# Kernel tuning notes

Measured on AMD Instinct MI355X. Metric: run time of the kernel, lower is better.

The kernel has to match this reference:

```python
import jax, jax.numpy as jnp
import numpy as np

EMBED_DIM = 2048
NUM_HEADS = 16
HEAD_DIM = EMBED_DIM // NUM_HEADS
BATCH = 4
SEQ = 1024
ROPE_BASE = 10000.0


def _rotate_half(x):
    x1, x2 = jnp.split(x, 2, axis=-1)
    return jnp.concatenate([-x2, x1], axis=-1)


def setup_inputs() -> dict:
    key = jax.random.key(0)
    ks = jax.random.split(key, 8)
    query = jax.random.normal(ks[0], (BATCH, SEQ, EMBED_DIM), dtype=jnp.float32)
    kkey = jax.random.normal(ks[1], (BATCH, SEQ, EMBED_DIM), dtype=jnp.float32)
    value = jax.random.normal(ks[2], (BATCH, SEQ, EMBED_DIM), dtype=jnp.float32)
    # causal mask: scores.masked_fill(mask == 0, -inf)
    mask = jnp.tril(jnp.ones((SEQ, SEQ), dtype=jnp.int32))[None, None]
    # RoPE tables [S, head_dim]
    inv_freq = 1.0 / (ROPE_BASE ** (np.arange(0, HEAD_DIM, 2, dtype=np.float32) / HEAD_DIM))
    pos = np.arange(SEQ, dtype=np.float32)
    freqs = np.outer(pos, inv_freq)                      # [S, D/2]
    emb = np.concatenate([freqs, freqs], axis=-1)        # [S, D]
    rope_cos = jnp.asarray(np.cos(emb), dtype=jnp.float32)
    rope_sin = jnp.asarray(np.sin(emb), dtype=jnp.float32)
    s = 1.0 / np.sqrt(EMBED_DIM)
    Wq = jax.random.normal(ks[3], (EMBED_DIM, EMBED_DIM), dtype=jnp.float32) * s
    Wk = jax.random.normal(ks[4], (EMBED_DIM, EMBED_DIM), dtype=jnp.float32) * s
    Wv = jax.random.normal(ks[5], (EMBED_DIM, EMBED_DIM), dtype=jnp.float32) * s
    Wo = jax.random.normal(ks[6], (EMBED_DIM, EMBED_DIM), dtype=jnp.float32) * s
    return {"query": query, "key": kkey, "value": value, "mask": mask,
            "rope_cos": rope_cos, "rope_sin": rope_sin,
            "Wq": Wq, "Wk": Wk, "Wv": Wv, "Wo": Wo}


def reference(query, key, value, mask, rope_cos, rope_sin, Wq, Wk, Wv, Wo):
    B, S, E = query.shape
    # projections (nn.Linear: x @ W.T)
    def proj(x, W):
        y = x @ W.T
        return y.reshape(B, -1, NUM_HEADS, HEAD_DIM).transpose(0, 2, 1, 3)  # [B,H,S,D]
    Q = proj(query, Wq)
    K = proj(key, Wk)
    V = proj(value, Wv)
    # RoPE (rotate-half form), cos/sin broadcast over batch and heads
    cos = rope_cos[None, None]  # [1,1,S,D]
    sin = rope_sin[None, None]
    Q = Q * cos + _rotate_half(Q) * sin
    K = K * cos + _rotate_half(K) * sin
    scale = jnp.asarray(np.sqrt(HEAD_DIM), dtype=Q.dtype)
    scores = jnp.einsum('bhqd,bhkd->bhqk', Q, K) / scale
    scores = jnp.where(mask == 0, jnp.asarray(-jnp.inf, scores.dtype), scores)
    attn = jax.nn.softmax(scores, axis=-1)
    context = jnp.einsum('bhqk,bhkd->bhqd', attn, V)
    context = context.transpose(0, 2, 1, 3).reshape(B, S, E)
    out = context @ Wo.T
    return out
```

## Files before the change

kernel.cpp:

```cpp
#include <hip/hip_runtime.h>
#include <stdint.h>

#define E_DIM 2048
#define N_HEADS 16
#define H_DIM 128
#define BATCH 4
#define SEQL 1024
#define M_ROWS 4096

typedef __attribute__((ext_vector_type(8))) short bf16x8;
typedef __attribute__((ext_vector_type(4))) float f32x4;

#define AS1 __attribute__((address_space(1)))
#define AS3 __attribute__((address_space(3)))

__device__ __forceinline__ void gload16(const void* g, void* l) {
  __builtin_amdgcn_global_load_lds((const AS1 uint32_t*)g, (AS3 uint32_t*)l, 16, 0, 0);
}

__device__ __forceinline__ unsigned short f2bf(float f) {
  union { float f; uint32_t u; } v; v.f = f;
  return (unsigned short)((v.u + 0x7FFFu + ((v.u >> 16) & 1u)) >> 16);
}

__global__ __launch_bounds__(256) void k_cvt(
    const float* __restrict__ q, const float* __restrict__ k, const float* __restrict__ v,
    const float* __restrict__ wq, const float* __restrict__ wk,
    const float* __restrict__ wv, const float* __restrict__ wo,
    ushort* __restrict__ oq, ushort* __restrict__ ok, ushort* __restrict__ ov,
    ushort* __restrict__ owq, ushort* __restrict__ owk,
    ushort* __restrict__ owv, ushort* __restrict__ owo) {
  int y = blockIdx.y;
  const float* in;
  ushort* out;
  if (y < 3) {
    in = (y == 0) ? q : (y == 1) ? k : v;
    out = (y == 0) ? oq : (y == 1) ? ok : ov;
  } else {
    if (blockIdx.x >= 4096) return;
    in = (y == 3) ? wq : (y == 4) ? wk : (y == 5) ? wv : wo;
    out = (y == 3) ? owq : (y == 4) ? owk : (y == 5) ? owv : owo;
  }
  int i = (blockIdx.x * 256 + threadIdx.x) * 4;
  float4 vv = *reinterpret_cast<const float4*>(in + i);
  *reinterpret_cast<ushort4*>(out + i) =
      make_ushort4(f2bf(vv.x), f2bf(vv.y), f2bf(vv.z), f2bf(vv.w));
}

template <int NREP>
__device__ __forceinline__ void gemm256_mainloop(const ushort* __restrict__ A,
                                                 const ushort* __restrict__ W,
                                                 ushort* lds, int m0, int n0,
                                                 const int browRows[NREP],
                                                 f32x4 (&acc)[8][NREP]) {
  const int tid = threadIdx.x;
  const int w = tid >> 6, lane = tid & 63, quad = lane >> 4, lid = lane & 15;
  constexpr int KTILES = E_DIM / 64;
  constexpr int BELE = NREP * 4096;
  ushort* const bufA = lds;
  ushort* const bufB = lds + 3 * 16384;

  const int r0 = tid >> 3, c0 = (tid & 7) ^ (r0 & 7);
  const int ldw = w * 512;
  const ushort* aB = A + ((size_t)m0 + r0) * E_DIM + c0 * 8;
  const ushort* bB = W + ((size_t)n0 + r0) * E_DIM + c0 * 8;

#define STG(baseP, buf, kt, half)                                              \
  do {                                                                         \
    const ushort* _g = (baseP) + (size_t)(half) * 128 * E_DIM + (kt) * 64;     \
    gload16(_g, (buf) + (half) * 8192 + ldw);                                  \
    gload16(_g + (size_t)64 * E_DIM, (buf) + (half) * 8192 + 4096 + ldw);      \
  } while (0)

  int ofsA[2], ofsB[NREP][2];
  {
    const int rowA = (w >> 2) * 128 + lid;
#pragma unroll
    for (int ks = 0; ks < 2; ++ks)
      ofsA[ks] = rowA * 64 + (((ks * 4 + quad) ^ (lid & 7)) * 8);
#pragma unroll
    for (int ni = 0; ni < NREP; ++ni)
#pragma unroll
      for (int ks = 0; ks < 2; ++ks)
        ofsB[ni][ks] = browRows[ni] * 64 + (((ks * 4 + quad) ^ (lid & 7)) * 8);
  }

  bf16x8 bfr[NREP][2];

#define VMW_STEADY                                                             \
  do {                                                                         \
    if constexpr (NREP == 4)                                                   \
      asm volatile("s_waitcnt vmcnt(8)" ::: "memory");                         \
    else                                                                       \
      asm volatile("s_waitcnt vmcnt(6)" ::: "memory");                         \
  } while (0)

#define PH(aoff, boff, q, STGS, VMW)                                           \
  do {                                                                         \
    bf16x8 af[2][2];                                                           \
    if ((q) == 0) {                                                            \
      _Pragma("unroll") for (int ni = 0; ni < NREP; ++ni)                      \
          _Pragma("unroll") for (int ks = 0; ks < 2; ++ks)                     \
              bfr[ni][ks] = *reinterpret_cast<const bf16x8*>(                  \
                  bufB + (boff) + ofsB[ni][ks]);                               \
    }                                                                          \
    _Pragma("unroll") for (int d = 0; d < 2; ++d)                              \
        _Pragma("unroll") for (int ks = 0; ks < 2; ++ks)                       \
            af[d][ks] = *reinterpret_cast<const bf16x8*>(                      \
                bufA + (aoff) + ofsA[ks] + ((q) * 2 + d) * 1024);              \
    STGS;                                                                      \
    VMW;                                                                       \
    __builtin_amdgcn_s_barrier();                                              \
    asm volatile("s_waitcnt lgkmcnt(0)" ::: "memory");                         \
    __builtin_amdgcn_s_setprio(1);                                             \
    _Pragma("unroll") for (int ks = 0; ks < 2; ++ks)                           \
        _Pragma("unroll") for (int d = 0; d < 2; ++d)                          \
            _Pragma("unroll") for (int ni = 0; ni < NREP; ++ni)                \
                acc[(q) * 2 + d][ni] = __builtin_amdgcn_mfma_f32_16x16x32_bf16(\
                    af[d][ks], bfr[ni][ks], acc[(q) * 2 + d][ni], 0, 0, 0);    \
    __builtin_amdgcn_s_setprio(0);                                             \
    __builtin_amdgcn_s_barrier();                                              \
  } while (0)

  STG(aB, bufA, 0, 0); STG(aB, bufA, 0, 1);
  STG(bB, bufB, 0, 0); if (NREP == 4) STG(bB, bufB, 0, 1);
  STG(aB, bufA + 16384, 1, 0); STG(aB, bufA + 16384, 1, 1);
  STG(bB, bufB + BELE, 1, 0); if (NREP == 4) STG(bB, bufB + BELE, 1, 1);
  VMW_STEADY;
  __builtin_amdgcn_s_barrier();

  int cur = 0, nx2 = 2;
  for (int t = 0; t < KTILES; ++t) {
    const int aoff = cur * 16384;
    const int boff = (t & 1) * BELE;
    ushort* sA = bufA + nx2 * 16384;
    ushort* sB = bufB + boff;
    const bool st = (t < KTILES - 2);
    PH(aoff, boff, 0, if (st) STG(aB, sA, t + 2, 0), );
    PH(aoff, boff, 1, if (st) STG(aB, sA, t + 2, 1), );
    PH(aoff, boff, 2, if (st) STG(bB, sB, t + 2, 0), );
    PH(aoff, boff, 3, if (st && NREP == 4) STG(bB, sB, t + 2, 1),
       if (st) VMW_STEADY;
       else if (t == KTILES - 2)
           asm volatile("s_waitcnt vmcnt(0)" ::: "memory"));
    cur = (cur == 2) ? 0 : cur + 1;
    nx2 = (nx2 == 2) ? 0 : nx2 + 1;
  }
#undef PH
#undef VMW_STEADY
#undef STG
}

__global__ __launch_bounds__(512, 2) void k_gemm_qkv(
    const ushort* __restrict__ xq, const ushort* __restrict__ xk, const ushort* __restrict__ xv,
    const ushort* __restrict__ wq, const ushort* __restrict__ wk, const ushort* __restrict__ wv,
    ushort* __restrict__ Qr, ushort* __restrict__ Kr, ushort* __restrict__ Vr,
    const float* __restrict__ cosT, const float* __restrict__ sinT) {
  extern __shared__ ushort lds[];
  unsigned lin = blockIdx.x + 8u * (blockIdx.y + 16u * blockIdx.z);
  unsigned swz = (lin & 7u) * 48u + (lin >> 3);
  const int bx = swz & 7u;
  const int by = (swz >> 3) & 15u;
  const int z = swz >> 7;

  const ushort* A = (z == 0) ? xq : (z == 1) ? xk : xv;
  const ushort* W = (z == 0) ? wq : (z == 1) ? wk : wv;
  ushort* Out = (z == 0) ? Qr : (z == 1) ? Kr : Vr;
  const int tid = threadIdx.x;
  const int w = tid >> 6, lane = tid & 63, quad = lane >> 4, lid = lane & 15;
  const int wn = w & 3;
  const int n0 = bx * 256;
  const int m0 = by * 256;

  int browRows[4];
#pragma unroll
  for (int ni = 0; ni < 4; ++ni)
    browRows[ni] = (wn >> 1) * 128 + (wn & 1) * 32 + (ni & 1) * 16 + (ni >> 1) * 64 + lid;

  f32x4 acc[8][4];
  const f32x4 z4 = {0.f, 0.f, 0.f, 0.f};
#pragma unroll
  for (int i = 0; i < 8; ++i)
#pragma unroll
    for (int j = 0; j < 4; ++j) acc[i][j] = z4;

  gemm256_mainloop<4>(A, W, lds, m0, n0, browRows, acc);

  const int b = m0 >> 10;
  const int h = bx * 2 + (wn >> 1);
  ushort* Og = Out + (size_t)(b * N_HEADS + h) * SEQL * H_DIM;
  const bool rope = (z < 2);
#pragma unroll
  for (int mi = 0; mi < 8; ++mi)
#pragma unroll
    for (int r = 0; r < 4; ++r) {
      int s = (m0 & (SEQL - 1)) + (w >> 2) * 128 + mi * 16 + quad * 4 + r;
      size_t row = (size_t)s * H_DIM;
      if (rope) {
#pragma unroll
        for (int ni = 0; ni < 2; ++ni) {
          int d0 = (wn & 1) * 32 + ni * 16 + lid;
          float c = cosT[s * H_DIM + d0];
          float sn = sinT[s * H_DIM + d0];
          float x0 = acc[mi][ni][r], x1 = acc[mi][ni + 2][r];
          Og[row + d0]      = f2bf(x0 * c - x1 * sn);
          Og[row + d0 + 64] = f2bf(x1 * c + x0 * sn);
        }
      } else {
#pragma unroll
        for (int ni = 0; ni < 4; ++ni) {
          int d = (wn & 1) * 32 + (ni & 1) * 16 + (ni >> 1) * 64 + lid;
          Og[row + d] = f2bf(acc[mi][ni][r]);
        }
      }
    }
}

__global__ __launch_bounds__(512, 2) void k_gemm_o(const ushort* __restrict__ A,
                                                   const ushort* __restrict__ W,
                                                   float* __restrict__ Out) {
  extern __shared__ ushort lds[];
  unsigned lin = blockIdx.x + 16u * blockIdx.y;
  unsigned swz = (lin & 7u) * 32u + (lin >> 3);
  const int bx = swz & 15u;
  const int by = swz >> 4;

  const int tid = threadIdx.x;
  const int w = tid >> 6, lane = tid & 63, quad = lane >> 4, lid = lane & 15;
  const int wn = w & 3;
  const int n0 = bx * 128;
  const int m0 = by * 256;

  int browRows[2];
#pragma unroll
  for (int ni = 0; ni < 2; ++ni) browRows[ni] = wn * 32 + ni * 16 + lid;

  f32x4 acc[8][2];
  const f32x4 z4 = {0.f, 0.f, 0.f, 0.f};
#pragma unroll
  for (int i = 0; i < 8; ++i)
#pragma unroll
    for (int j = 0; j < 2; ++j) acc[i][j] = z4;

  gemm256_mainloop<2>(A, W, lds, m0, n0, browRows, acc);

#pragma unroll
  for (int mi = 0; mi < 8; ++mi)
#pragma unroll
    for (int r = 0; r < 4; ++r) {
      size_t row = (size_t)(m0 + (w >> 2) * 128 + mi * 16 + quad * 4 + r) * E_DIM + n0;
#pragma unroll
      for (int ni = 0; ni < 2; ++ni) Out[row + browRows[ni]] = acc[mi][ni][r];
    }
}

__global__ __launch_bounds__(256) void k_transv(const ushort* __restrict__ V,
                                                ushort* __restrict__ Vt) {
  __shared__ ushort t[32][33];
  int bh = blockIdx.z;
  int s0 = blockIdx.x * 32;
  int d0 = blockIdx.y * 32;
  int j = threadIdx.x & 31;
  int i = threadIdx.x >> 5;
  for (int rr = 0; rr < 4; ++rr) {
    int row = i + rr * 8;
    t[row][j] = V[((size_t)bh * SEQL + s0 + row) * H_DIM + d0 + j];
  }
  __syncthreads();
  for (int rr = 0; rr < 4; ++rr) {
    int drow = i + rr * 8;
    Vt[((size_t)bh * H_DIM + d0 + drow) * SEQL + s0 + j] = t[j][drow];
  }
}

__global__ __launch_bounds__(256, 2) void k_attn(const ushort* __restrict__ Q,
                                                 const ushort* __restrict__ K,
                                                 const ushort* __restrict__ Vt,
                                                 ushort* __restrict__ Ctx) {
  __shared__ ushort Ks[128 * 128];
  __shared__ ushort Vs[128 * 64];
  __shared__ ushort Ps[4][32 * 40];
  const int tid = threadIdx.x;
  const int w = tid >> 6, lane = tid & 63, quad = lane >> 4, lid = lane & 15;
  const int l = blockIdx.y * 8 + blockIdx.x;
  const int bh = l & 63;
  const int slot = l >> 6;
  const int qt = (slot < 4) ? slot : 11 - slot;
  const int q0 = qt * 128;
  const size_t base = (size_t)bh * SEQL * H_DIM;
  const ushort* Qg = Q + base;
  const ushort* Kg = K + base;
  const ushort* Vg = Vt + base;

  bf16x8 qf[2][4];
  for (int mt = 0; mt < 2; ++mt) {
    int row = q0 + w * 32 + mt * 16 + lid;
    for (int kc = 0; kc < 4; ++kc)
      qf[mt][kc] = *reinterpret_cast<const bf16x8*>(Qg + (size_t)row * H_DIM + kc * 32 + quad * 8);
  }

  f32x4 oacc[2][8];
  f32x4 lacc[2];
  const f32x4 z4 = {0.f, 0.f, 0.f, 0.f};
  for (int mt = 0; mt < 2; ++mt) {
    lacc[mt] = z4;
    for (int dt = 0; dt < 8; ++dt) oacc[mt][dt] = z4;
  }

  bf16x8 ones;
  for (int i = 0; i < 8; ++i) ones[i] = (short)0x3F80;

  const float SC2 = 0.08838834764831845f * 1.4426950408889634f;
  const float M2 = 12.0f * 1.4426950408889634f;

  for (int j0 = 0; j0 <= q0; j0 += 128) {
    const bool diag = (j0 == q0);
    __syncthreads();
    for (int i = 0; i < 8; ++i) {
      int g = i * 256 + tid;
      int kk = g >> 4;
      int c = (g & 15) ^ (kk & 15);
      gload16(Kg + (size_t)(j0 + kk) * H_DIM + c * 8, Ks + (i * 256 + w * 64) * 8);
    }
    for (int i = 0; i < 4; ++i) {
      int g = i * 256 + tid;
      int d = g >> 3;
      int c = (g & 7) ^ (d & 7);
      gload16(Vg + (size_t)d * SEQL + j0 + c * 8, Vs + (i * 256 + w * 64) * 8);
    }
    __syncthreads();

    f32x4 sacc[2][8];
    for (int mt = 0; mt < 2; ++mt)
      for (int nt = 0; nt < 8; ++nt) sacc[mt][nt] = z4;
    for (int kc = 0; kc < 4; ++kc)
      for (int nt = 0; nt < 8; ++nt) {
        int kk = nt * 16 + lid;
        bf16x8 kf = *reinterpret_cast<const bf16x8*>(
            Ks + kk * H_DIM + (((kc * 4 + quad) ^ lid) * 8));
        sacc[0][nt] = __builtin_amdgcn_mfma_f32_16x16x32_bf16(qf[0][kc], kf, sacc[0][nt], 0, 0, 0);
        sacc[1][nt] = __builtin_amdgcn_mfma_f32_16x16x32_bf16(qf[1][kc], kf, sacc[1][nt], 0, 0, 0);
      }

    if (diag) {
      for (int mt = 0; mt < 2; ++mt)
        for (int nt = 0; nt < 8; ++nt)
          for (int r = 0; r < 4; ++r) {
            int key = j0 + nt * 16 + lid;
            int row = q0 + w * 32 + mt * 16 + quad * 4 + r;
            if (key > row) sacc[mt][nt][r] = -3.0e38f;
          }
    }

    ushort* Pw = Ps[w];
    for (int kc = 0; kc < 4; ++kc) {
      if (kc == 2) {
        __syncthreads();
        for (int i = 0; i < 4; ++i) {
          int g = i * 256 + tid;
          int d = g >> 3;
          int c = (g & 7) ^ (d & 7);
          gload16(Vg + (size_t)d * SEQL + j0 + 64 + c * 8, Vs + (i * 256 + w * 64) * 8);
        }
        __syncthreads();
      }
      for (int mt = 0; mt < 2; ++mt)
        for (int half = 0; half < 2; ++half) {
          int nt = kc * 2 + half;
          for (int r = 0; r < 4; ++r) {
            float p = exp2f(fmaf(sacc[mt][nt][r], SC2, -M2));
            Pw[(mt * 16 + quad * 4 + r) * 40 + half * 16 + lid] = f2bf(p);
          }
        }
      bf16x8 pf0 = *reinterpret_cast<const bf16x8*>(Pw + lid * 40 + quad * 8);
      bf16x8 pf1 = *reinterpret_cast<const bf16x8*>(Pw + (16 + lid) * 40 + quad * 8);
      lacc[0] = __builtin_amdgcn_mfma_f32_16x16x32_bf16(pf0, ones, lacc[0], 0, 0, 0);
      lacc[1] = __builtin_amdgcn_mfma_f32_16x16x32_bf16(pf1, ones, lacc[1], 0, 0, 0);
      int kcl = kc & 1;
      for (int dt = 0; dt < 8; ++dt) {
        int d = dt * 16 + lid;
        bf16x8 vf = *reinterpret_cast<const bf16x8*>(
            Vs + d * 64 + (((kcl * 4 + quad) ^ (d & 7)) * 8));
        oacc[0][dt] = __builtin_amdgcn_mfma_f32_16x16x32_bf16(pf0, vf, oacc[0][dt], 0, 0, 0);
        oacc[1][dt] = __builtin_amdgcn_mfma_f32_16x16x32_bf16(pf1, vf, oacc[1][dt], 0, 0, 0);
      }
    }
  }

  const int b = bh >> 4, h = bh & 15;
  for (int mt = 0; mt < 2; ++mt)
    for (int r = 0; r < 4; ++r) {
      int s = q0 + w * 32 + mt * 16 + quad * 4 + r;
      float inv = 1.0f / lacc[mt][r];
      for (int dt = 0; dt < 8; ++dt)
        Ctx[(size_t)(b * SEQL + s) * E_DIM + h * H_DIM + dt * 16 + lid] =
            f2bf(oacc[mt][dt][r] * inv);
    }
}

extern "C" void kernel_launch(void* const* d_in, const int* in_sizes, int n_in,
                              void* d_out, int out_size, void* d_ws, size_t ws_size,
                              hipStream_t stream) {
  const float* q_in = (const float*)d_in[0];
  const float* k_in = (const float*)d_in[1];
  const float* v_in = (const float*)d_in[2];
  const float* rc = (const float*)d_in[4];
  const float* rs = (const float*)d_in[5];
  const float* Wq = (const float*)d_in[6];
  const float* Wk = (const float*)d_in[7];
  const float* Wv = (const float*)d_in[8];
  const float* Wo = (const float*)d_in[9];
  float* out = (float*)d_out;

  ushort* p = (ushort*)d_ws;
  const size_t WSZ = (size_t)E_DIM * E_DIM;
  const size_t XSZ = (size_t)M_ROWS * E_DIM;
  ushort* wq_b = p; p += WSZ;
  ushort* wk_b = p; p += WSZ;
  ushort* wv_b = p; p += WSZ;
  ushort* wo_b = p; p += WSZ;
  ushort* xq_b = p; p += XSZ;
  ushort* xk_b = p; p += XSZ;
  ushort* xv_b = p; p += XSZ;
  ushort* Qr = p;   p += XSZ;
  ushort* Kr = p;   p += XSZ;
  ushort* Vr = p;   p += XSZ;
  ushort* Vt = p;   p += XSZ;
  ushort* ctx = xq_b;

  (void)hipFuncSetAttribute(reinterpret_cast<const void*>(k_gemm_qkv),
                            hipFuncAttributeMaxDynamicSharedMemorySize, 163840);
  (void)hipFuncSetAttribute(reinterpret_cast<const void*>(k_gemm_o),
                            hipFuncAttributeMaxDynamicSharedMemorySize, 131072);

  dim3 blk(256);
  k_cvt<<<dim3(8192, 7), blk, 0, stream>>>(q_in, k_in, v_in, Wq, Wk, Wv, Wo,
                                           xq_b, xk_b, xv_b, wq_b, wk_b, wv_b, wo_b);

  k_gemm_qkv<<<dim3(E_DIM / 256, M_ROWS / 256, 3), dim3(512), 163840, stream>>>(
      xq_b, xk_b, xv_b, wq_b, wk_b, wv_b, Qr, Kr, Vr, rc, rs);

  k_transv<<<dim3(SEQL / 32, H_DIM / 32, BATCH * N_HEADS), blk, 0, stream>>>(Vr, Vt);

  k_attn<<<dim3(8, BATCH * N_HEADS), blk, 0, stream>>>(Qr, Kr, Vt, ctx);

  k_gemm_o<<<dim3(E_DIM / 128, M_ROWS / 256), dim3(512), 131072, stream>>>(ctx, wo_b, out);
}
```

Measured before the change: 423.7 us.

## Switch GEMMs to double buffering, drop tile swizzle, double-buffer attention K/V

The GEMM mainloop goes from a triple-buffered A pipeline to double-buffered A and B with a 2x unrolled loop and tighter vmcnt waits, which cuts the LDS footprint of both GEMMs. The block-index swizzle for L2 locality is removed from both GEMM kernels. The attention kernel moves to dynamic LDS holding full 128-wide K and V tiles, double-buffered, so the next tile prefetches during compute and the mid-loop V reload with its extra barriers goes away. In exchange there is less prefetch depth in the GEMMs, possibly worse cache locality without the swizzle, and a large attention LDS allocation that limits it to one block per CU.

```diff
diff --git a/kernel.cpp b/kernel.cpp
--- a/kernel.cpp
+++ b/kernel.cpp
@@ -55,22 +55,26 @@
                                                  f32x4 (&acc)[8][NREP]) {
   const int tid = threadIdx.x;
   const int w = tid >> 6, lane = tid & 63, quad = lane >> 4, lid = lane & 15;
-  constexpr int KTILES = E_DIM / 64;
   constexpr int BELE = NREP * 4096;
-  ushort* const bufA = lds;
-  ushort* const bufB = lds + 3 * 16384;
-
-  const int r0 = tid >> 3, c0 = (tid & 7) ^ (r0 & 7);
-  const int ldw = w * 512;
-  const ushort* aB = A + ((size_t)m0 + r0) * E_DIM + c0 * 8;
-  const ushort* bB = W + ((size_t)n0 + r0) * E_DIM + c0 * 8;
-
-#define STG(baseP, buf, kt, half)                                              \
-  do {                                                                         \
-    const ushort* _g = (baseP) + (size_t)(half) * 128 * E_DIM + (kt) * 64;     \
-    gload16(_g, (buf) + (half) * 8192 + ldw);                                  \
-    gload16(_g + (size_t)64 * E_DIM, (buf) + (half) * 8192 + 4096 + ldw);      \
-  } while (0)
+  ushort* bufA[2] = {lds, lds + 16384};
+  ushort* bufB[2] = {lds + 32768, lds + 32768 + BELE};
+
+  const int p0 = tid, p1i = tid + 512;
+  const int r0 = p0 >> 3, c0 = (p0 & 7) ^ (r0 & 7);
+  const int r1 = p1i >> 3, c1 = (p1i & 7) ^ (r1 & 7);
+  const int ld0 = (w * 64) * 8;
+  const int ld1 = (512 + w * 64) * 8;
+
+  const ushort* gA = A + (size_t)m0 * E_DIM;
+  const ushort* gB = W + (size_t)n0 * E_DIM;
+
+  auto stage = [&](const ushort* g, ushort* buf, int kt, int half) {
+    const ushort* s0p = g + (size_t)(half * 128 + r0) * E_DIM + kt * 64 + c0 * 8;
+    const ushort* s1p = g + (size_t)(half * 128 + r1) * E_DIM + kt * 64 + c1 * 8;
+    ushort* l = buf + half * 8192;
+    gload16(s0p, l + ld0);
+    gload16(s1p, l + ld1);
+  };
 
   int ofsA[2], ofsB[NREP][2];
   {
@@ -87,27 +91,27 @@
 
   bf16x8 bfr[NREP][2];
 
-#define VMW_STEADY                                                             \
+#define VMW_N                                                                  \
   do {                                                                         \
     if constexpr (NREP == 4)                                                   \
-      asm volatile("s_waitcnt vmcnt(8)" ::: "memory");                         \
+      asm volatile("s_waitcnt vmcnt(4)" ::: "memory");                         \
     else                                                                       \
-      asm volatile("s_waitcnt vmcnt(6)" ::: "memory");                         \
+      asm volatile("s_waitcnt vmcnt(2)" ::: "memory");                         \
   } while (0)
 
-#define PH(aoff, boff, q, STGS, VMW)                                           \
+#define PH(b, q, STGS, VMW)                                                    \
   do {                                                                         \
     bf16x8 af[2][2];                                                           \
     if ((q) == 0) {                                                            \
       _Pragma("unroll") for (int ni = 0; ni < NREP; ++ni)                      \
           _Pragma("unroll") for (int ks = 0; ks < 2; ++ks)                     \
-              bfr[ni][ks] = *reinterpret_cast<const bf16x8*>(                  \
-                  bufB + (boff) + ofsB[ni][ks]);                               \
+              bfr[ni][ks] =                                                    \
+                  *reinterpret_cast<const bf16x8*>(bufB[b] + ofsB[ni][ks]);    \
     }                                                                          \
     _Pragma("unroll") for (int d = 0; d < 2; ++d)                              \
         _Pragma("unroll") for (int ks = 0; ks < 2; ++ks)                       \
             af[d][ks] = *reinterpret_cast<const bf16x8*>(                      \
-                bufA + (aoff) + ofsA[ks] + ((q) * 2 + d) * 1024);              \
+                bufA[b] + ofsA[ks] + ((q) * 2 + d) * 1024);                    \
     STGS;                                                                      \
     VMW;                                                                       \
     __builtin_amdgcn_s_barrier();                                              \
@@ -122,33 +126,29 @@
     __builtin_amdgcn_s_barrier();                                              \
   } while (0)
 
-  STG(aB, bufA, 0, 0); STG(aB, bufA, 0, 1);
-  STG(bB, bufB, 0, 0); if (NREP == 4) STG(bB, bufB, 0, 1);
-  STG(aB, bufA + 16384, 1, 0); STG(aB, bufA + 16384, 1, 1);
-  STG(bB, bufB + BELE, 1, 0); if (NREP == 4) STG(bB, bufB + BELE, 1, 1);
-  VMW_STEADY;
+  stage(gB, bufB[0], 0, 0); if (NREP == 4) stage(gB, bufB[0], 0, 1);
+  stage(gA, bufA[0], 0, 0); stage(gA, bufA[0], 0, 1);
+  stage(gB, bufB[1], 1, 0); if (NREP == 4) stage(gB, bufB[1], 1, 1);
+  VMW_N;
   __builtin_amdgcn_s_barrier();
 
-  int cur = 0, nx2 = 2;
-  for (int t = 0; t < KTILES; ++t) {
-    const int aoff = cur * 16384;
-    const int boff = (t & 1) * BELE;
-    ushort* sA = bufA + nx2 * 16384;
-    ushort* sB = bufB + boff;
-    const bool st = (t < KTILES - 2);
-    PH(aoff, boff, 0, if (st) STG(aB, sA, t + 2, 0), );
-    PH(aoff, boff, 1, if (st) STG(aB, sA, t + 2, 1), );
-    PH(aoff, boff, 2, if (st) STG(bB, sB, t + 2, 0), );
-    PH(aoff, boff, 3, if (st && NREP == 4) STG(bB, sB, t + 2, 1),
-       if (st) VMW_STEADY;
-       else if (t == KTILES - 2)
-           asm volatile("s_waitcnt vmcnt(0)" ::: "memory"));
-    cur = (cur == 2) ? 0 : cur + 1;
-    nx2 = (nx2 == 2) ? 0 : nx2 + 1;
+  for (int i = 0; i < 16; ++i) {
+    const bool lastI = (i == 15);
+    const int tn = 2 * i;
+    PH(0, 0, stage(gA, bufA[1], tn + 1, 0), );
+    PH(0, 1, stage(gA, bufA[1], tn + 1, 1), );
+    PH(0, 2, if (!lastI) stage(gB, bufB[0], tn + 2, 0), );
+    PH(0, 3, if (!lastI && NREP == 4) stage(gB, bufB[0], tn + 2, 1),
+       if (lastI) asm volatile("s_waitcnt vmcnt(0)" ::: "memory");
+       else VMW_N);
+    PH(1, 0, if (!lastI) stage(gA, bufA[0], tn + 2, 0), );
+    PH(1, 1, if (!lastI) stage(gA, bufA[0], tn + 2, 1), );
+    PH(1, 2, if (!lastI) stage(gB, bufB[1], tn + 3, 0), );
+    PH(1, 3, if (!lastI && NREP == 4) stage(gB, bufB[1], tn + 3, 1),
+       if (!lastI) VMW_N);
   }
 #undef PH
-#undef VMW_STEADY
-#undef STG
+#undef VMW_N
 }
 
 __global__ __launch_bounds__(512, 2) void k_gemm_qkv(
@@ -157,20 +157,15 @@
     ushort* __restrict__ Qr, ushort* __restrict__ Kr, ushort* __restrict__ Vr,
     const float* __restrict__ cosT, const float* __restrict__ sinT) {
   extern __shared__ ushort lds[];
-  unsigned lin = blockIdx.x + 8u * (blockIdx.y + 16u * blockIdx.z);
-  unsigned swz = (lin & 7u) * 48u + (lin >> 3);
-  const int bx = swz & 7u;
-  const int by = (swz >> 3) & 15u;
-  const int z = swz >> 7;
-
+  const int z = blockIdx.z;
   const ushort* A = (z == 0) ? xq : (z == 1) ? xk : xv;
   const ushort* W = (z == 0) ? wq : (z == 1) ? wk : wv;
   ushort* Out = (z == 0) ? Qr : (z == 1) ? Kr : Vr;
   const int tid = threadIdx.x;
   const int w = tid >> 6, lane = tid & 63, quad = lane >> 4, lid = lane & 15;
   const int wn = w & 3;
-  const int n0 = bx * 256;
-  const int m0 = by * 256;
+  const int n0 = blockIdx.x * 256;
+  const int m0 = blockIdx.y * 256;
 
   int browRows[4];
 #pragma unroll
@@ -187,7 +182,7 @@
   gemm256_mainloop<4>(A, W, lds, m0, n0, browRows, acc);
 
   const int b = m0 >> 10;
-  const int h = bx * 2 + (wn >> 1);
+  const int h = blockIdx.x * 2 + (wn >> 1);
   ushort* Og = Out + (size_t)(b * N_HEADS + h) * SEQL * H_DIM;
   const bool rope = (z < 2);
 #pragma unroll
@@ -220,16 +215,11 @@
                                                    const ushort* __restrict__ W,
                                                    float* __restrict__ Out) {
   extern __shared__ ushort lds[];
-  unsigned lin = blockIdx.x + 16u * blockIdx.y;
-  unsigned swz = (lin & 7u) * 32u + (lin >> 3);
-  const int bx = swz & 15u;
-  const int by = swz >> 4;
-
   const int tid = threadIdx.x;
   const int w = tid >> 6, lane = tid & 63, quad = lane >> 4, lid = lane & 15;
   const int wn = w & 3;
-  const int n0 = bx * 128;
-  const int m0 = by * 256;
+  const int n0 = blockIdx.x * 128;
+  const int m0 = blockIdx.y * 256;
 
   int browRows[2];
 #pragma unroll
@@ -273,15 +263,15 @@
   }
 }
 
-__global__ __launch_bounds__(256, 2) void k_attn(const ushort* __restrict__ Q,
-                                                 const ushort* __restrict__ K,
-                                                 const ushort* __restrict__ Vt,
-                                                 ushort* __restrict__ Ctx) {
-  __shared__ ushort Ks[128 * 128];
-  __shared__ ushort Vs[128 * 64];
-  __shared__ ushort Ps[4][32 * 40];
+__global__ __launch_bounds__(256) void k_attn(const ushort* __restrict__ Q,
+                                              const ushort* __restrict__ K,
+                                              const ushort* __restrict__ Vt,
+                                              ushort* __restrict__ Ctx) {
+  extern __shared__ ushort lds[];
   const int tid = threadIdx.x;
   const int w = tid >> 6, lane = tid & 63, quad = lane >> 4, lid = lane & 15;
+  ushort* Pw = lds + 65536 + w * 1280;
+
   const int l = blockIdx.y * 8 + blockIdx.x;
   const int bh = l & 63;
   const int slot = l >> 6;
@@ -292,6 +282,25 @@
   const ushort* Kg = K + base;
   const ushort* Vg = Vt + base;
 
+  auto stageK = [&](ushort* dst, int j0) {
+#pragma unroll
+    for (int i = 0; i < 8; ++i) {
+      int g = i * 256 + tid;
+      int kk = g >> 4;
+      int c = (g & 15) ^ (kk & 15);
+      gload16(Kg + (size_t)(j0 + kk) * H_DIM + c * 8, dst + (i * 256 + w * 64) * 8);
+    }
+  };
+  auto stageV = [&](ushort* dst, int j0) {
+#pragma unroll
+    for (int i = 0; i < 8; ++i) {
+      int g = i * 256 + tid;
+      int d = g >> 4;
+      int c = (g & 15) ^ (d & 15);
+      gload16(Vg + (size_t)d * SEQL + j0 + c * 8, dst + (i * 256 + w * 64) * 8);
+    }
+  };
+
   bf16x8 qf[2][4];
   for (int mt = 0; mt < 2; ++mt) {
     int row = q0 + w * 32 + mt * 16 + lid;
@@ -313,22 +322,16 @@
   const float SC2 = 0.08838834764831845f * 1.4426950408889634f;
   const float M2 = 12.0f * 1.4426950408889634f;
 
+  ushort *Kc = lds, *Kn = lds + 16384;
+  ushort *Vc = lds + 32768, *Vn = lds + 49152;
+
+  stageK(Kc, 0);
+  stageV(Vc, 0);
+  __syncthreads();
+
   for (int j0 = 0; j0 <= q0; j0 += 128) {
     const bool diag = (j0 == q0);
-    __syncthreads();
-    for (int i = 0; i < 8; ++i) {
-      int g = i * 256 + tid;
-      int kk = g >> 4;
-      int c = (g & 15) ^ (kk & 15);
-      gload16(Kg + (size_t)(j0 + kk) * H_DIM + c * 8, Ks + (i * 256 + w * 64) * 8);
-    }
-    for (int i = 0; i < 4; ++i) {
-      int g = i * 256 + tid;
-      int d = g >> 3;
-      int c = (g & 7) ^ (d & 7);
-      gload16(Vg + (size_t)d * SEQL + j0 + c * 8, Vs + (i * 256 + w * 64) * 8);
-    }
-    __syncthreads();
+    if (!diag) { stageK(Kn, j0 + 128); stageV(Vn, j0 + 128); }
 
     f32x4 sacc[2][8];
     for (int mt = 0; mt < 2; ++mt)
@@ -337,7 +340,7 @@
       for (int nt = 0; nt < 8; ++nt) {
         int kk = nt * 16 + lid;
         bf16x8 kf = *reinterpret_cast<const bf16x8*>(
-            Ks + kk * H_DIM + (((kc * 4 + quad) ^ lid) * 8));
+            Kc + kk * H_DIM + (((kc * 4 + quad) ^ lid) * 8));
         sacc[0][nt] = __builtin_amdgcn_mfma_f32_16x16x32_bf16(qf[0][kc], kf, sacc[0][nt], 0, 0, 0);
         sacc[1][nt] = __builtin_amdgcn_mfma_f32_16x16x32_bf16(qf[1][kc], kf, sacc[1][nt], 0, 0, 0);
       }
@@ -352,18 +355,7 @@
           }
     }
 
-    ushort* Pw = Ps[w];
     for (int kc = 0; kc < 4; ++kc) {
-      if (kc == 2) {
-        __syncthreads();
-        for (int i = 0; i < 4; ++i) {
-          int g = i * 256 + tid;
-          int d = g >> 3;
-          int c = (g & 7) ^ (d & 7);
-          gload16(Vg + (size_t)d * SEQL + j0 + 64 + c * 8, Vs + (i * 256 + w * 64) * 8);
-        }
-        __syncthreads();
-      }
       for (int mt = 0; mt < 2; ++mt)
         for (int half = 0; half < 2; ++half) {
           int nt = kc * 2 + half;
@@ -376,15 +368,18 @@
       bf16x8 pf1 = *reinterpret_cast<const bf16x8*>(Pw + (16 + lid) * 40 + quad * 8);
       lacc[0] = __builtin_amdgcn_mfma_f32_16x16x32_bf16(pf0, ones, lacc[0], 0, 0, 0);
       lacc[1] = __builtin_amdgcn_mfma_f32_16x16x32_bf16(pf1, ones, lacc[1], 0, 0, 0);
-      int kcl = kc & 1;
       for (int dt = 0; dt < 8; ++dt) {
         int d = dt * 16 + lid;
         bf16x8 vf = *reinterpret_cast<const bf16x8*>(
-            Vs + d * 64 + (((kcl * 4 + quad) ^ (d & 7)) * 8));
+            Vc + d * 128 + (((kc * 4 + quad) ^ (d & 15)) * 8));
         oacc[0][dt] = __builtin_amdgcn_mfma_f32_16x16x32_bf16(pf0, vf, oacc[0][dt], 0, 0, 0);
         oacc[1][dt] = __builtin_amdgcn_mfma_f32_16x16x32_bf16(pf1, vf, oacc[1][dt], 0, 0, 0);
       }
     }
+
+    __syncthreads();
+    ushort* t0 = Kc; Kc = Kn; Kn = t0;
+    ushort* t1 = Vc; Vc = Vn; Vn = t1;
   }
 
   const int b = bh >> 4, h = bh & 15;
@@ -429,20 +424,22 @@
   ushort* ctx = xq_b;
 
   (void)hipFuncSetAttribute(reinterpret_cast<const void*>(k_gemm_qkv),
-                            hipFuncAttributeMaxDynamicSharedMemorySize, 163840);
+                            hipFuncAttributeMaxDynamicSharedMemorySize, 131072);
   (void)hipFuncSetAttribute(reinterpret_cast<const void*>(k_gemm_o),
-                            hipFuncAttributeMaxDynamicSharedMemorySize, 131072);
+                            hipFuncAttributeMaxDynamicSharedMemorySize, 98304);
+  (void)hipFuncSetAttribute(reinterpret_cast<const void*>(k_attn),
+                            hipFuncAttributeMaxDynamicSharedMemorySize, 141312);
 
   dim3 blk(256);
   k_cvt<<<dim3(8192, 7), blk, 0, stream>>>(q_in, k_in, v_in, Wq, Wk, Wv, Wo,
                                            xq_b, xk_b, xv_b, wq_b, wk_b, wv_b, wo_b);
 
-  k_gemm_qkv<<<dim3(E_DIM / 256, M_ROWS / 256, 3), dim3(512), 163840, stream>>>(
+  k_gemm_qkv<<<dim3(E_DIM / 256, M_ROWS / 256, 3), dim3(512), 131072, stream>>>(
       xq_b, xk_b, xv_b, wq_b, wk_b, wv_b, Qr, Kr, Vr, rc, rs);
 
   k_transv<<<dim3(SEQL / 32, H_DIM / 32, BATCH * N_HEADS), blk, 0, stream>>>(Vr, Vt);
 
-  k_attn<<<dim3(8, BATCH * N_HEADS), blk, 0, stream>>>(Qr, Kr, Vt, ctx);
-
-  k_gemm_o<<<dim3(E_DIM / 128, M_ROWS / 256), dim3(512), 131072, stream>>>(ctx, wo_b, out);
-}
+  k_attn<<<dim3(8, BATCH * N_HEADS), blk, 141312, stream>>>(Qr, Kr, Vt, ctx);
+
+  k_gemm_o<<<dim3(E_DIM / 128, M_ROWS / 256), dim3(512), 98304, stream>>>(ctx, wo_b, out);
+}
```

Result: faster. 408.4 us (-3.6%).
